# Optimization experiments

Hardware: AMD Instinct MI355X
Metric: run time of the kernel (lower is better)

The kernel has to match this reference:

```python
import math
import jax, jax.numpy as jnp
import numpy as np

GRID_SIZE = 17
GRID_RANGE = 2.5
WIDTHS = [128, 256, 128]
LN_EPS = 1e-5

GRID = jnp.linspace(-GRID_RANGE, GRID_RANGE, GRID_SIZE, dtype=jnp.float32)
SPACING = jnp.float32(2.0 * GRID_RANGE / (GRID_SIZE - 1))


def _kan_layer(x, base_scale, spline_w, bias):
    # x: (B, I); base_scale: (I, O); spline_w: (I, O, G); bias: (O,)
    I = x.shape[-1]
    # degree-1 (hat) spline basis: (B, I, G)
    basis = jnp.clip(1.0 - jnp.abs(x[..., None] - GRID) / SPACING, 0.0, None)
    spline = jnp.einsum('big,iog->bio', basis, spline_w)          # (B, I, O)
    base = jax.nn.silu(x)[..., None] * base_scale[None]            # (B, I, O)
    edge = base + spline                                           # (B, I, O)
    out = edge.sum(axis=1) / math.sqrt(float(I)) + bias            # (B, O)
    return out, edge, basis


def _layer_norm(x, gamma, beta):
    mu = x.mean(axis=-1, keepdims=True)
    var = ((x - mu) ** 2).mean(axis=-1, keepdims=True)
    return (x - mu) * jax.lax.rsqrt(var + LN_EPS) * gamma + beta


def setup_inputs() -> dict:
    key = jax.random.key(0)
    ks = jax.random.split(key, 8)
    B = 4096
    I0, H, O = WIDTHS
    fan0 = 1.0 / math.sqrt(float(I0))
    fan1 = 1.0 / math.sqrt(float(H))
    return {
        'x': jax.random.normal(ks[0], (B, I0), dtype=jnp.float32),
        'base_scale0': fan0 * jax.random.normal(ks[1], (I0, H), dtype=jnp.float32),
        'spline_w0': 0.1 * fan0 * jax.random.normal(ks[2], (I0, H, GRID_SIZE), dtype=jnp.float32),
        'bias0': jnp.zeros((H,), dtype=jnp.float32),
        'base_scale1': fan1 * jax.random.normal(ks[3], (H, O), dtype=jnp.float32),
        'spline_w1': 0.1 * fan1 * jax.random.normal(ks[4], (H, O, GRID_SIZE), dtype=jnp.float32),
        'bias1': jnp.zeros((O,), dtype=jnp.float32),
        'ln_gamma': jnp.ones((H,), dtype=jnp.float32),
        'ln_beta': jnp.zeros((H,), dtype=jnp.float32),
    }


def reference(x, base_scale0, spline_w0, bias0, base_scale1, spline_w1, bias1, ln_gamma, ln_beta):
    h, _, _ = _kan_layer(x, base_scale0, spline_w0, bias0)
    h = _layer_norm(h, ln_gamma, ln_beta)
    out, edge1, basis1 = _kan_layer(h, base_scale1, spline_w1, bias1)
    # diagnostics on the last layer (mean/std, std unbiased=False)
    se_mean = edge1.mean()
    se_std = edge1.std()
    sb_mean = basis1.mean()
    sb_std = basis1.std()
    return out, edge1, basis1, se_mean, se_std, sb_mean, sb_std
```

## Files before the change

kernel.cpp:

```cpp
#include <hip/hip_runtime.h>

#define BATCH 4096
#define NI 128
#define NH 256
#define NO 128
#define NG 17

static constexpr size_t EDGE_OFF  = (size_t)BATCH * NO;
static constexpr size_t BASIS_OFF = EDGE_OFF + (size_t)BATCH * NH * NO;
static constexpr size_t SCAL_OFF  = BASIS_OFF + (size_t)BATCH * NH * NG;

typedef float  vf2 __attribute__((ext_vector_type(2)));
typedef float  vf4 __attribute__((ext_vector_type(4)));

__device__ __forceinline__ unsigned short f2bf(float v) {
    unsigned int b = __float_as_uint(v);
    b += 0x7FFFu + ((b >> 16) & 1u);
    return (unsigned short)(b >> 16);
}
__device__ __forceinline__ float bf2f(unsigned short u) {
    return __uint_as_float((unsigned int)u << 16);
}
__device__ __forceinline__ float4 bf4_to_f4(uint2 v) {
    float4 r;
    r.x = __uint_as_float(v.x << 16);
    r.y = __uint_as_float(v.x & 0xFFFF0000u);
    r.z = __uint_as_float(v.y << 16);
    r.w = __uint_as_float(v.y & 0xFFFF0000u);
    return r;
}

__device__ __forceinline__ void taps(float v, float& sil, float& wlo, float& whi,
                                     int& glo, int& ghi, float& u) {
    sil = v / (1.0f + __expf(-v));
    u   = (v + 2.5f) * 3.2f;
    float kf = floorf(u);
    int   k  = (int)kf;
    float f  = u - kf;
    wlo = 1.0f - f;  whi = f;
    glo = k;         ghi = k + 1;
    if (glo < 0 || glo > 16) { glo = 0; wlo = 0.0f; }
    if (ghi < 0 || ghi > 16) { ghi = 0; whi = 0.0f; }
}

__global__ __launch_bounds__(256) void transpose_convert(
    const float* __restrict__ w0, const float* __restrict__ w1,
    const float* __restrict__ bs1,
    unsigned short* __restrict__ w0t, unsigned short* __restrict__ w1t,
    unsigned short* __restrict__ bs1b) {
    int j = blockIdx.x * 256 + threadIdx.x;
    const int total0 = NI * NG * NH;
    const int total1 = NH * NG * NO;
    if (j < total0) {
        int i = j / (NG * NH);
        int r = j - i * (NG * NH);
        int g = r / NH;
        int o = r - g * NH;
        w0t[j] = f2bf(w0[((size_t)i * NH + o) * NG + g]);
    } else if (j < total0 + total1) {
        int jj = j - total0;
        int i = jj / (NG * NO);
        int r = jj - i * (NG * NO);
        int g = r / NO;
        int o = r - g * NO;
        w1t[jj] = f2bf(w1[((size_t)i * NO + o) * NG + g]);
    } else {
        int jj = j - total0 - total1;
        bs1b[jj] = f2bf(bs1[jj]);
    }
}

__global__ __launch_bounds__(128) void kan_fused(
    const float* __restrict__ x,
    const float* __restrict__ bs0,
    const float* __restrict__ bias0,
    const unsigned short* __restrict__ bs1,
    const float* __restrict__ bias1,
    const float* __restrict__ gamma,
    const float* __restrict__ beta,
    const unsigned short* __restrict__ w0t,
    const unsigned short* __restrict__ w1t,
    float* __restrict__ out,
    float4* __restrict__ partials)
{
    __shared__ float s_sil0[NI], s_wlo0[NI], s_whi0[NI];
    __shared__ int   s_glo0[NI], s_ghi0[NI];
    __shared__ float s_sil1[NH], s_wlo1[NH], s_whi1[NH], s_u1[NH];
    __shared__ int   s_glo1[NH], s_ghi1[NH];
    __shared__ float s_red[128];
    __shared__ float4 s_out4[128];
    __shared__ float4 s_red4[128];

    const int tid = threadIdx.x;
    const int b   = blockIdx.x;

    {
        float xv = x[(size_t)b * NI + tid];
        float sil, wlo, whi, u; int glo, ghi;
        taps(xv, sil, wlo, whi, glo, ghi, u);
        s_sil0[tid] = sil; s_wlo0[tid] = wlo; s_whi0[tid] = whi;
        s_glo0[tid] = glo; s_ghi0[tid] = ghi;
    }
    __syncthreads();

    float h0 = 0.0f, h1 = 0.0f;
    for (int i = 0; i < NI; ++i) {
        const float sil = s_sil0[i], wlo = s_wlo0[i], whi = s_whi0[i];
        const float* bsr = bs0 + (size_t)i * NH;
        const unsigned short* wl = w0t + (size_t)(i * NG + s_glo0[i]) * NH;
        const unsigned short* wh = w0t + (size_t)(i * NG + s_ghi0[i]) * NH;
        h0 += sil * bsr[tid]       + wlo * bf2f(wl[tid])       + whi * bf2f(wh[tid]);
        h1 += sil * bsr[tid + 128] + wlo * bf2f(wl[tid + 128]) + whi * bf2f(wh[tid + 128]);
    }
    h0 = h0 * 0.08838834764831844f + bias0[tid];
    h1 = h1 * 0.08838834764831844f + bias0[tid + 128];

    s_red[tid] = h0 + h1;
    __syncthreads();
    for (int s = 64; s > 0; s >>= 1) {
        if (tid < s) s_red[tid] += s_red[tid + s];
        __syncthreads();
    }
    const float mu = s_red[0] * (1.0f / NH);
    __syncthreads();
    const float d0 = h0 - mu, d1 = h1 - mu;
    s_red[tid] = d0 * d0 + d1 * d1;
    __syncthreads();
    for (int s = 64; s > 0; s >>= 1) {
        if (tid < s) s_red[tid] += s_red[tid + s];
        __syncthreads();
    }
    const float rs = rsqrtf(s_red[0] * (1.0f / NH) + 1e-5f);
    __syncthreads();
    const float hn0 = d0 * rs * gamma[tid]       + beta[tid];
    const float hn1 = d1 * rs * gamma[tid + 128] + beta[tid + 128];

    float bsum, bsq;
    {
        float sil, wlo, whi, u; int glo, ghi;
        taps(hn0, sil, wlo, whi, glo, ghi, u);
        s_sil1[tid] = sil; s_wlo1[tid] = wlo; s_whi1[tid] = whi;
        s_glo1[tid] = glo; s_ghi1[tid] = ghi; s_u1[tid] = u;
        bsum = wlo + whi;  bsq = wlo * wlo + whi * whi;
        taps(hn1, sil, wlo, whi, glo, ghi, u);
        s_sil1[tid + 128] = sil; s_wlo1[tid + 128] = wlo; s_whi1[tid + 128] = whi;
        s_glo1[tid + 128] = glo; s_ghi1[tid + 128] = ghi; s_u1[tid + 128] = u;
        bsum += wlo + whi; bsq += wlo * wlo + whi * whi;
    }
    __syncthreads();

    {
        float* bo = out + BASIS_OFF + (size_t)b * (NH * NG);
        #pragma unroll
        for (int it = 0; it < 17; ++it) {
            int j2 = it * 128 + tid;
            int f0 = j2 * 2;
            int i0 = f0 / NG,       g0 = f0 - i0 * NG;
            int i1 = (f0 + 1) / NG, g1 = (f0 + 1) - i1 * NG;
            vf2 v;
            v.x = fmaxf(0.0f, 1.0f - fabsf(s_u1[i0] - (float)g0));
            v.y = fmaxf(0.0f, 1.0f - fabsf(s_u1[i1] - (float)g1));
            __builtin_nontemporal_store(v, reinterpret_cast<vf2*>(bo + f0));
        }
    }

    const int po = (tid & 31) * 4;
    const int q  = tid >> 5;
    float4 osum = make_float4(0.f, 0.f, 0.f, 0.f);
    float esq = 0.0f;
    float* eo = out + EDGE_OFF + (size_t)b * (NH * NO);
    #pragma unroll 2
    for (int it = 0; it < 64; ++it) {
        const int i = q * 64 + it;
        const float sil = s_sil1[i], wlo = s_wlo1[i], whi = s_whi1[i];
        const float4 bsv = bf4_to_f4(*reinterpret_cast<const uint2*>(bs1 + (size_t)i * NO + po));
        const float4 wl  = bf4_to_f4(*reinterpret_cast<const uint2*>(w1t + (size_t)(i * NG + s_glo1[i]) * NO + po));
        const float4 wh  = bf4_to_f4(*reinterpret_cast<const uint2*>(w1t + (size_t)(i * NG + s_ghi1[i]) * NO + po));
        vf4 e;
        e.x = sil * bsv.x + wlo * wl.x + whi * wh.x;
        e.y = sil * bsv.y + wlo * wl.y + whi * wh.y;
        e.z = sil * bsv.z + wlo * wl.z + whi * wh.z;
        e.w = sil * bsv.w + wlo * wl.w + whi * wh.w;
        __builtin_nontemporal_store(e, reinterpret_cast<vf4*>(eo + (size_t)i * NO + po));
        osum.x += e.x; osum.y += e.y; osum.z += e.z; osum.w += e.w;
        esq += e.x * e.x + e.y * e.y + e.z * e.z + e.w * e.w;
    }

    s_out4[tid] = osum;
    __syncthreads();
    if (tid < 32) {
        float4 a = s_out4[tid], b2 = s_out4[tid + 32], c = s_out4[tid + 64], d2 = s_out4[tid + 96];
        const float4 bi = *reinterpret_cast<const float4*>(bias1 + tid * 4);
        float4 o4;
        o4.x = (a.x + b2.x + c.x + d2.x) * 0.0625f + bi.x;
        o4.y = (a.y + b2.y + c.y + d2.y) * 0.0625f + bi.y;
        o4.z = (a.z + b2.z + c.z + d2.z) * 0.0625f + bi.z;
        o4.w = (a.w + b2.w + c.w + d2.w) * 0.0625f + bi.w;
        *reinterpret_cast<float4*>(out + (size_t)b * NO + tid * 4) = o4;
    }

    s_red4[tid] = make_float4(osum.x + osum.y + osum.z + osum.w, esq, bsum, bsq);
    __syncthreads();
    for (int s = 64; s > 0; s >>= 1) {
        if (tid < s) {
            float4 a = s_red4[tid], c = s_red4[tid + s];
            s_red4[tid] = make_float4(a.x + c.x, a.y + c.y, a.z + c.z, a.w + c.w);
        }
        __syncthreads();
    }
    if (tid == 0) partials[b] = s_red4[0];
}

__global__ __launch_bounds__(256) void finalize(const float4* __restrict__ partials,
                                                float* __restrict__ out) {
    __shared__ double red[256];
    const int tid = threadIdx.x;
    double a0 = 0, a1 = 0, a2 = 0, a3 = 0;
    for (int j = tid; j < BATCH; j += 256) {
        float4 p = partials[j];
        a0 += (double)p.x; a1 += (double)p.y; a2 += (double)p.z; a3 += (double)p.w;
    }
    double tot[4];
    double v[4] = {a0, a1, a2, a3};
    for (int c = 0; c < 4; ++c) {
        red[tid] = v[c];
        __syncthreads();
        for (int s = 128; s > 0; s >>= 1) {
            if (tid < s) red[tid] += red[tid + s];
            __syncthreads();
        }
        tot[c] = red[0];
        __syncthreads();
    }
    if (tid == 0) {
        const double Ne = (double)BATCH * NH * NO;
        const double Nb = (double)BATCH * NH * NG;
        double me = tot[0] / Ne;
        double ve = tot[1] / Ne - me * me;
        double mb = tot[2] / Nb;
        double vb = tot[3] / Nb - mb * mb;
        out[SCAL_OFF + 0] = (float)me;
        out[SCAL_OFF + 1] = (float)sqrt(ve > 0.0 ? ve : 0.0);
        out[SCAL_OFF + 2] = (float)mb;
        out[SCAL_OFF + 3] = (float)sqrt(vb > 0.0 ? vb : 0.0);
    }
}

extern "C" void kernel_launch(void* const* d_in, const int* in_sizes, int n_in,
                              void* d_out, int out_size, void* d_ws, size_t ws_size,
                              hipStream_t stream) {
    const float* x     = (const float*)d_in[0];
    const float* bs0   = (const float*)d_in[1];
    const float* w0    = (const float*)d_in[2];
    const float* bias0 = (const float*)d_in[3];
    const float* bs1   = (const float*)d_in[4];
    const float* w1    = (const float*)d_in[5];
    const float* bias1 = (const float*)d_in[6];
    const float* gamma = (const float*)d_in[7];
    const float* beta  = (const float*)d_in[8];
    float* out = (float*)d_out;

    unsigned short* w0t  = (unsigned short*)d_ws;
    unsigned short* w1t  = w0t + (size_t)NI * NG * NH;
    unsigned short* bs1b = w1t + (size_t)NH * NG * NO;
    size_t ofs = ((size_t)(NI * NG * NH) + (size_t)(NH * NG * NO) + NH * NO) * sizeof(unsigned short);
    ofs = (ofs + 15) & ~(size_t)15;
    float4* partials = (float4*)((char*)d_ws + ofs);

    hipLaunchKernelGGL(transpose_convert, dim3(4480), dim3(256), 0, stream,
                       w0, w1, bs1, w0t, w1t, bs1b);
    hipLaunchKernelGGL(kan_fused, dim3(BATCH), dim3(128), 0, stream,
                       x, bs0, bias0, bs1b, bias1, gamma, beta, w0t, w1t, out, partials);
    hipLaunchKernelGGL(finalize, dim3(1), dim3(256), 0, stream, partials, out);
}
```

Measured before the change: 164.0 us.

## Split layer 0 into a batched kernel that stages weights in shared memory

Layer 0 moves out of the per-row fused kernel into its own kernel. Each 512-thread block handles 16 batch rows and stages tiles of bf16 spline weights and base scales in LDS, so each weight fetch from global memory is reused across 16 rows instead of one. LayerNorm statistics are computed with wave shuffles using a single-pass sum and sum of squares. The normalized hidden activations pass to the layer-1 kernel through a global workspace buffer, which adds a kernel launch and a round trip through memory. The one-pass variance formula may also lose some precision.

```diff
diff --git a/kernel.cpp b/kernel.cpp
--- a/kernel.cpp
+++ b/kernel.cpp
@@ -5,6 +5,8 @@
 #define NH 256
 #define NO 128
 #define NG 17
+#define RROWS 16
+#define TI 4
 
 static constexpr size_t EDGE_OFF  = (size_t)BATCH * NO;
 static constexpr size_t BASIS_OFF = EDGE_OFF + (size_t)BATCH * NH * NO;
@@ -70,70 +72,125 @@
     }
 }
 
-__global__ __launch_bounds__(128) void kan_fused(
+__global__ __launch_bounds__(512) void kan_layer0(
     const float* __restrict__ x,
     const float* __restrict__ bs0,
     const float* __restrict__ bias0,
-    const unsigned short* __restrict__ bs1,
-    const float* __restrict__ bias1,
     const float* __restrict__ gamma,
     const float* __restrict__ beta,
     const unsigned short* __restrict__ w0t,
+    float* __restrict__ hn)
+{
+    __shared__ unsigned short s_w0[TI * NG * NH];
+    __shared__ float  s_bs0[TI * NH];
+    __shared__ float  s_x[RROWS * NI];
+    __shared__ float  s_taps[RROWS * TI * 4];
+    __shared__ float2 s_lnp[8][8];
+    __shared__ float2 s_mv[RROWS];
+
+    const int tid  = threadIdx.x;
+    const int o    = tid & 255;
+    const int half = tid >> 8;
+    const int rb   = blockIdx.x * RROWS;
+
+    for (int j = tid; j < RROWS * NI; j += 512) s_x[j] = x[(size_t)rb * NI + j];
+
+    const float b0 = bias0[o];
+    const float gm = gamma[o];
+    const float bt = beta[o];
+
+    float acc[8];
+    #pragma unroll
+    for (int k = 0; k < 8; ++k) acc[k] = 0.0f;
+
+    for (int t = 0; t < NI / TI; ++t) {
+        const int i0 = t * TI;
+        __syncthreads();
+        {
+            const unsigned int* src = (const unsigned int*)(w0t + (size_t)i0 * NG * NH);
+            unsigned int* dst = (unsigned int*)s_w0;
+            #pragma unroll
+            for (int k = 0; k < 17; ++k) dst[tid + k * 512] = src[tid + k * 512];
+        }
+        {
+            const float* src = bs0 + (size_t)i0 * NH;
+            s_bs0[tid] = src[tid];
+            s_bs0[tid + 512] = src[tid + 512];
+        }
+        if (tid < RROWS * TI) {
+            const int r  = tid >> 2;
+            const int il = tid & 3;
+            float xv = s_x[r * NI + i0 + il];
+            float sil, wlo, whi, u; int glo, ghi;
+            taps(xv, sil, wlo, whi, glo, ghi, u);
+            s_taps[tid * 4 + 0] = sil;
+            s_taps[tid * 4 + 1] = wlo;
+            s_taps[tid * 4 + 2] = whi;
+            s_taps[tid * 4 + 3] = __int_as_float(glo | (ghi << 8));
+        }
+        __syncthreads();
+        #pragma unroll
+        for (int il = 0; il < TI; ++il) {
+            const float bsv = s_bs0[il * NH + o];
+            const unsigned short* wbase = s_w0 + il * NG * NH;
+            #pragma unroll
+            for (int r8 = 0; r8 < 8; ++r8) {
+                const int rr = half * 8 + r8;
+                const int ti = (rr * TI + il) * 4;
+                const float sil = s_taps[ti], wlo = s_taps[ti + 1], whi = s_taps[ti + 2];
+                const unsigned int gp = __float_as_uint(s_taps[ti + 3]);
+                const float wl = bf2f(wbase[(gp & 0xffu) * NH + o]);
+                const float wh = bf2f(wbase[(gp >> 8) * NH + o]);
+                acc[r8] += sil * bsv + wlo * wl + whi * wh;
+            }
+        }
+    }
+
+    float h[8];
+    #pragma unroll
+    for (int r8 = 0; r8 < 8; ++r8) {
+        h[r8] = acc[r8] * 0.08838834764831844f + b0;
+        float s = h[r8], q = h[r8] * h[r8];
+        #pragma unroll
+        for (int d = 1; d < 64; d <<= 1) { s += __shfl_xor(s, d, 64); q += __shfl_xor(q, d, 64); }
+        if ((tid & 63) == 0) s_lnp[tid >> 6][r8] = make_float2(s, q);
+    }
+    __syncthreads();
+    if (tid < RROWS) {
+        const int bw = (tid >> 3) * 4, r8 = tid & 7;
+        float2 a = s_lnp[bw][r8], b2 = s_lnp[bw + 1][r8], c = s_lnp[bw + 2][r8], d = s_lnp[bw + 3][r8];
+        float sm = a.x + b2.x + c.x + d.x, sq = a.y + b2.y + c.y + d.y;
+        float mu = sm * (1.0f / NH);
+        float var = sq * (1.0f / NH) - mu * mu;
+        s_mv[tid] = make_float2(mu, rsqrtf(var + 1e-5f));
+    }
+    __syncthreads();
+    #pragma unroll
+    for (int r8 = 0; r8 < 8; ++r8) {
+        const int rr = half * 8 + r8;
+        float2 mv = s_mv[rr];
+        hn[(size_t)(rb + rr) * NH + o] = (h[r8] - mv.x) * mv.y * gm + bt;
+    }
+}
+
+__global__ __launch_bounds__(128) void kan_layer1(
+    const float* __restrict__ hn,
+    const unsigned short* __restrict__ bs1,
+    const float* __restrict__ bias1,
     const unsigned short* __restrict__ w1t,
     float* __restrict__ out,
     float4* __restrict__ partials)
 {
-    __shared__ float s_sil0[NI], s_wlo0[NI], s_whi0[NI];
-    __shared__ int   s_glo0[NI], s_ghi0[NI];
     __shared__ float s_sil1[NH], s_wlo1[NH], s_whi1[NH], s_u1[NH];
     __shared__ int   s_glo1[NH], s_ghi1[NH];
-    __shared__ float s_red[128];
     __shared__ float4 s_out4[128];
     __shared__ float4 s_red4[128];
 
     const int tid = threadIdx.x;
     const int b   = blockIdx.x;
 
-    {
-        float xv = x[(size_t)b * NI + tid];
-        float sil, wlo, whi, u; int glo, ghi;
-        taps(xv, sil, wlo, whi, glo, ghi, u);
-        s_sil0[tid] = sil; s_wlo0[tid] = wlo; s_whi0[tid] = whi;
-        s_glo0[tid] = glo; s_ghi0[tid] = ghi;
-    }
-    __syncthreads();
-
-    float h0 = 0.0f, h1 = 0.0f;
-    for (int i = 0; i < NI; ++i) {
-        const float sil = s_sil0[i], wlo = s_wlo0[i], whi = s_whi0[i];
-        const float* bsr = bs0 + (size_t)i * NH;
-        const unsigned short* wl = w0t + (size_t)(i * NG + s_glo0[i]) * NH;
-        const unsigned short* wh = w0t + (size_t)(i * NG + s_ghi0[i]) * NH;
-        h0 += sil * bsr[tid]       + wlo * bf2f(wl[tid])       + whi * bf2f(wh[tid]);
-        h1 += sil * bsr[tid + 128] + wlo * bf2f(wl[tid + 128]) + whi * bf2f(wh[tid + 128]);
-    }
-    h0 = h0 * 0.08838834764831844f + bias0[tid];
-    h1 = h1 * 0.08838834764831844f + bias0[tid + 128];
-
-    s_red[tid] = h0 + h1;
-    __syncthreads();
-    for (int s = 64; s > 0; s >>= 1) {
-        if (tid < s) s_red[tid] += s_red[tid + s];
-        __syncthreads();
-    }
-    const float mu = s_red[0] * (1.0f / NH);
-    __syncthreads();
-    const float d0 = h0 - mu, d1 = h1 - mu;
-    s_red[tid] = d0 * d0 + d1 * d1;
-    __syncthreads();
-    for (int s = 64; s > 0; s >>= 1) {
-        if (tid < s) s_red[tid] += s_red[tid + s];
-        __syncthreads();
-    }
-    const float rs = rsqrtf(s_red[0] * (1.0f / NH) + 1e-5f);
-    __syncthreads();
-    const float hn0 = d0 * rs * gamma[tid]       + beta[tid];
-    const float hn1 = d1 * rs * gamma[tid + 128] + beta[tid + 128];
+    const float hn0 = hn[(size_t)b * NH + tid];
+    const float hn1 = hn[(size_t)b * NH + tid + 128];
 
     float bsum, bsq;
     {
@@ -266,10 +323,13 @@
     size_t ofs = ((size_t)(NI * NG * NH) + (size_t)(NH * NG * NO) + NH * NO) * sizeof(unsigned short);
     ofs = (ofs + 15) & ~(size_t)15;
     float4* partials = (float4*)((char*)d_ws + ofs);
+    float*  hnbuf    = (float*)((char*)d_ws + ofs + BATCH * sizeof(float4));
 
     hipLaunchKernelGGL(transpose_convert, dim3(4480), dim3(256), 0, stream,
                        w0, w1, bs1, w0t, w1t, bs1b);
-    hipLaunchKernelGGL(kan_fused, dim3(BATCH), dim3(128), 0, stream,
-                       x, bs0, bias0, bs1b, bias1, gamma, beta, w0t, w1t, out, partials);
+    hipLaunchKernelGGL(kan_layer0, dim3(BATCH / RROWS), dim3(512), 0, stream,
+                       x, bs0, bias0, gamma, beta, w0t, hnbuf);
+    hipLaunchKernelGGL(kan_layer1, dim3(BATCH), dim3(128), 0, stream,
+                       hnbuf, bs1b, bias1, w1t, out, partials);
     hipLaunchKernelGGL(finalize, dim3(1), dim3(256), 0, stream, partials, out);
 }
```

After: 196.1 us. 1.2x slower.
